# Optimization experiments

Hardware: AMD Instinct MI355X
Metric: run time of the kernel (lower is better)

The kernel has to match this reference:

```python
import jax, jax.numpy as jnp
import numpy as np

N = 50000   # nodes
E = 800000  # edges
G = 64      # graphs in the batch
DIN = 128
DOUT = 256


def _lin(key, fan_in, fan_out):
    s = 1.0 / np.sqrt(fan_in)
    kw, kb = jax.random.split(key)
    W = jax.random.uniform(kw, (fan_in, fan_out), jnp.float32, -s, s)
    b = jax.random.uniform(kb, (fan_out,), jnp.float32, -s, s)
    return W, b


def setup_inputs() -> dict:
    key = jax.random.key(0)
    ks = jax.random.split(key, 12)
    x = jax.random.normal(ks[0], (N, DIN), jnp.float32)
    edge_index = jax.random.randint(ks[1], (2, E), 0, N, dtype=jnp.int64)
    batch = jnp.sort(jax.random.randint(ks[2], (N,), 0, G, dtype=jnp.int64))
    W1, b1 = _lin(ks[3], DIN, 128)
    W2, b2 = _lin(ks[4], 128, 128)
    W3, b3 = _lin(ks[5], 128, 128)
    A1, ba1 = _lin(ks[6], DIN, 64)
    A2, ba2 = _lin(ks[7], 64, 32)
    A3, ba3 = _lin(ks[8], 32, 1)
    M1, bm1 = _lin(ks[9], 128, 128)
    M2, bm2 = _lin(ks[10], 128, DOUT)
    return dict(x=x, edge_index=edge_index, batch=batch,
                W1=W1, b1=b1, W2=W2, b2=b2, W3=W3, b3=b3,
                A1=A1, ba1=ba1, A2=A2, ba2=ba2, A3=A3, ba3=ba3,
                M1=M1, bm1=bm1, M2=M2, bm2=bm2)


def _gcn_norm(edge_index, n, dtype):
    # GCNConv default: add self-loops, symmetric normalization D^-1/2 (A+I) D^-1/2
    loop = jnp.arange(n, dtype=edge_index.dtype)
    src = jnp.concatenate([edge_index[0], loop])
    dst = jnp.concatenate([edge_index[1], loop])
    deg = jax.ops.segment_sum(jnp.ones_like(dst, dtype), dst, num_segments=n)
    dinv = jnp.where(deg > 0, jax.lax.rsqrt(deg), 0.0)
    return src, dst, dinv[src] * dinv[dst]


def _gcn(h, W, b, src, dst, norm, n):
    h = h @ W                                   # [N, F_out]
    msg = h[src] * norm[:, None]                # gather + scale (memory bound)
    return jax.ops.segment_sum(msg, dst, num_segments=n) + b


def _segment_softmax(w, batch, g):
    # per-graph softmax (PyG softmax): stabilize with segment max
    m = jax.ops.segment_max(w, batch, num_segments=g)
    e = jnp.exp(w - m[batch])
    s = jax.ops.segment_sum(e, batch, num_segments=g)
    return e / (s[batch] + 1e-16)


def reference(x, edge_index, batch,
              W1, b1, W2, b2, W3, b3,
              A1, ba1, A2, ba2, A3, ba3,
              M1, bm1, M2, bm2):
    n = x.shape[0]
    src, dst, norm = _gcn_norm(edge_index, n, x.dtype)
    relu = jax.nn.relu
    # feature branch
    f = relu(_gcn(x, W1, b1, src, dst, norm, n))
    f = relu(_gcn(f, W2, b2, src, dst, norm, n))
    f = relu(_gcn(f, W3, b3, src, dst, norm, n))
    # attention branch
    w = relu(_gcn(x, A1, ba1, src, dst, norm, n))
    w = relu(_gcn(w, A2, ba2, src, dst, norm, n))
    w = relu(_gcn(w, A3, ba3, src, dst, norm, n))   # [N, 1]
    w = _segment_softmax(w, batch, G)
    # attention-weighted sum pooling per graph
    pooled = jax.ops.segment_sum(f * w, batch, num_segments=G)  # [G, 128]
    # MLP([128,128,256], batch_norm=False): Linear+ReLU, plain last Linear
    out = relu(pooled @ M1 + bm1) @ M2 + bm2
    return out
```

## Files before the change

kernel.cpp:

```cpp
#include <hip/hip_runtime.h>
#include <hip/hip_fp16.h>
#include <math.h>


#define DIN 128
#define FH  128
#define DOUT 256
#define NBUK 128
#define SUBN 512
#define IMGCAP 16384
#define ECAP 16384

typedef float f4 __attribute__((ext_vector_type(4)));
typedef float f32x4 __attribute__((ext_vector_type(4)));
typedef _Float16 h8v __attribute__((ext_vector_type(8)));
typedef _Float16 h4v __attribute__((ext_vector_type(4)));


__global__ __launch_bounds__(256) void scan1_kernel(const int* __restrict__ cnt,
        int* __restrict__ bsum, float* __restrict__ dinv, int n) {
    __shared__ int sm[256];
    int tid = threadIdx.x;
    int base = blockIdx.x * 512;
    int a = (base + tid < n) ? cnt[base + tid] : 0;
    int b = (base + 256 + tid < n) ? cnt[base + 256 + tid] : 0;
    if (base + tid < n)       dinv[base + tid]       = rsqrtf((float)(a + 1));
    if (base + 256 + tid < n) dinv[base + 256 + tid] = rsqrtf((float)(b + 1));
    sm[tid] = a + b;
    __syncthreads();
    for (int off = 128; off > 0; off >>= 1) {
        if (tid < off) sm[tid] += sm[tid + off];
        __syncthreads();
    }
    if (tid == 0) bsum[blockIdx.x] = sm[0];
}

__global__ void scan2_kernel(const int* __restrict__ bsum, int* __restrict__ boff,
                             int* __restrict__ rpN, int nb) {
    if (threadIdx.x == 0) {
        int run = 0;
        for (int i = 0; i < nb; ++i) { boff[i] = run; run += bsum[i]; }
        *rpN = run;
    }
}

__global__ __launch_bounds__(256) void scan3_kernel(const int* __restrict__ cnt,
        const int* __restrict__ boff, int* __restrict__ rp, int n) {
    __shared__ int sm[256];
    int tid = threadIdx.x;
    int base = blockIdx.x * 512;
    int i0 = base + 2 * tid;
    int c0 = (i0 < n) ? cnt[i0] : 0;
    int c1 = (i0 + 1 < n) ? cnt[i0 + 1] : 0;
    int ps = c0 + c1;
    sm[tid] = ps;
    __syncthreads();
    for (int off = 1; off < 256; off <<= 1) {
        int v = (tid >= off) ? sm[tid - off] : 0;
        __syncthreads();
        sm[tid] += v;
        __syncthreads();
    }
    int excl = sm[tid] - ps + boff[blockIdx.x];
    if (i0 < n) rp[i0] = excl;
    if (i0 + 1 < n) rp[i0 + 1] = excl + c0;
}

__global__ __launch_bounds__(256) void ebucket_kernel(const int* __restrict__ src,
        const int* __restrict__ dst, int* __restrict__ bcur,
        unsigned long long* __restrict__ entries, int E, int shift) {
    __shared__ int lcnt[NBUK], lscan[NBUK], lbase[NBUK], lcur[NBUK];
    __shared__ unsigned long long stage[2048];
    const int tid = threadIdx.x;
    const int e0 = blockIdx.x * 2048;
    if (tid < NBUK) { lcnt[tid] = 0; lcur[tid] = 0; }
    __syncthreads();
    int s_[8], d_[8];
    #pragma unroll
    for (int k = 0; k < 8; ++k) {
        int e = e0 + k * 256 + tid;
        if (e < E) {
            s_[k] = src[e];
            d_[k] = dst[e];
            atomicAdd(&lcnt[d_[k] >> shift], 1);
        } else {
            d_[k] = -1;
        }
    }
    __syncthreads();
    if (tid < NBUK) lscan[tid] = lcnt[tid];
    __syncthreads();
    for (int off = 1; off < NBUK; off <<= 1) {
        int v = 0;
        if (tid < NBUK && tid >= off) v = lscan[tid - off];
        __syncthreads();
        if (tid < NBUK) lscan[tid] += v;
        __syncthreads();
    }
    if (tid < NBUK) {
        lscan[tid] -= lcnt[tid];
        lbase[tid] = lcnt[tid] ? atomicAdd(&bcur[tid], lcnt[tid]) : 0;
    }
    __syncthreads();
    #pragma unroll
    for (int k = 0; k < 8; ++k) {
        if (d_[k] >= 0) {
            int b = d_[k] >> shift;
            int pos = lscan[b] + atomicAdd(&lcur[b], 1);
            stage[pos] = ((unsigned long long)(unsigned)d_[k] << 32) | (unsigned)s_[k];
        }
    }
    __syncthreads();
    const int total = min(2048, E - e0);
    for (int i = tid; i < total; i += 256) {
        int lo = 0, hi = NBUK - 1;
        while (lo < hi) {
            int mid = (lo + hi + 1) >> 1;
            if (lscan[mid] <= i) lo = mid; else hi = mid - 1;
        }
        int idx = lbase[lo] + (i - lscan[lo]);
        if (idx < (lo + 1) * ECAP)
            entries[(size_t)idx] = stage[i];
    }
}

__global__ __launch_bounds__(512) void ecount_kernel(
        const unsigned long long* __restrict__ entries,
        const int* __restrict__ bcur, int* __restrict__ cnt, int n, int shift) {
    __shared__ int hist[SUBN];
    const int b = blockIdx.x;
    const int n0 = b << shift;
    if (n0 >= n) return;
    const int n1 = min(n0 + SUBN, n);
    const int tid = threadIdx.x;
    hist[tid] = 0;
    __syncthreads();
    const size_t ebase = (size_t)b * ECAP;
    const int len = min(bcur[b] - b * ECAP, ECAP);
    for (int i = tid; i < len; i += 512)
        atomicAdd(&hist[(int)(entries[ebase + i] >> 32) - n0], 1);
    __syncthreads();
    if (n0 + tid < n1) cnt[n0 + tid] = hist[tid];
}

__global__ __launch_bounds__(512) void ecsr_kernel(
        const unsigned long long* __restrict__ entries,
        const int* __restrict__ rp, const float* __restrict__ dinv,
        long long* __restrict__ cn, int n, int shift) {
    __shared__ long long img[IMGCAP];
    __shared__ int hist[SUBN];
    __shared__ int lcur[SUBN];
    __shared__ int sm[SUBN];
    __shared__ float dl[SUBN];
    const int b = blockIdx.x;
    const int n0 = b << shift;
    if (n0 >= n) return;
    const int n1 = min(n0 + (1 << shift), n);
    const int base = rp[n0];
    const int len  = rp[n1] - base;
    const size_t ebase = (size_t)b * ECAP;
    const int tid = threadIdx.x;
    hist[tid] = 0;
    lcur[tid] = 0;
    if (n0 + tid < n1) dl[tid] = dinv[n0 + tid];
    __syncthreads();
    for (int i = tid; i < len; i += 512)
        atomicAdd(&hist[(int)(entries[ebase + i] >> 32) - n0], 1);
    __syncthreads();
    int v = hist[tid];
    sm[tid] = v;
    __syncthreads();
    for (int off = 1; off < SUBN; off <<= 1) {
        int t = (tid >= off) ? sm[tid - off] : 0;
        __syncthreads();
        sm[tid] += t;
        __syncthreads();
    }
    hist[tid] = sm[tid] - v;
    __syncthreads();
    const bool fits = (len <= IMGCAP);
    for (int i = tid; i < len; i += 512) {
        unsigned long long e = entries[ebase + i];
        int d  = (int)(e >> 32) - n0;
        int sx = (int)(unsigned)(e & 0xffffffffu);
        int pos = hist[d] + atomicAdd(&lcur[d], 1);
        float w = dinv[sx] * dl[d];
        long long val = (long long)(unsigned)sx | ((long long)__float_as_int(w) << 32);
        if (fits) img[pos] = val;
        else      cn[base + pos] = val;
    }
    __syncthreads();
    if (fits)
        for (int i = tid; i < len; i += 512) cn[base + i] = img[i];
}

__global__ void gstart_kernel(const int* __restrict__ batch, int* __restrict__ gstart,
                              int n, int g) {
    int t = threadIdx.x;
    if (t > g) return;
    int lo = 0, hi = n;
    while (lo < hi) {
        int mid = (lo + hi) >> 1;
        if (batch[mid] < t) lo = mid + 1; else hi = mid;
    }
    gstart[t] = lo;
}

__global__ void cvt16_kernel(const float* __restrict__ in, __half* __restrict__ outh,
                             long n8) {
    long i = (long)blockIdx.x * 256 + threadIdx.x;
    if (i >= n8) return;
    f4 a = ((const f4*)in)[2 * i];
    f4 b = ((const f4*)in)[2 * i + 1];
    __half2 h0 = __float22half2_rn(make_float2(a.x, a.y));
    __half2 h1 = __float22half2_rn(make_float2(a.z, a.w));
    __half2 h2 = __float22half2_rn(make_float2(b.x, b.y));
    __half2 h3 = __float22half2_rn(make_float2(b.z, b.w));
    uint4 st;
    st.x = *(unsigned*)&h0; st.y = *(unsigned*)&h1;
    st.z = *(unsigned*)&h2; st.w = *(unsigned*)&h3;
    ((uint4*)outh)[i] = st;
}


__device__ __forceinline__ void wsplit(const float* __restrict__ W,
        _Float16* __restrict__ Th, _Float16* __restrict__ Tl,
        int fin, int fout, int i) {
    int r = i / fout, c = i % fout;
    float w = W[i];
    _Float16 h = (_Float16)w;
    Th[c * fin + r] = h;
    Tl[c * fin + r] = (_Float16)(w - (float)h);
}

__global__ __launch_bounds__(256) void wprep_kernel(const float* __restrict__ W1,
        const float* __restrict__ W2, const float* __restrict__ W3,
        const float* __restrict__ A1, const float* __restrict__ A2,
        _Float16* __restrict__ T, int* __restrict__ bcur) {
    int i = blockIdx.x * 256 + threadIdx.x;
    if (blockIdx.x == 0 && threadIdx.x < NBUK) bcur[threadIdx.x] = threadIdx.x * ECAP;
    if (i < 16384)       wsplit(W1, T,          T + 16384,  128, 128, i);
    else if (i < 32768)  wsplit(W2, T + 32768,  T + 49152,  128, 128, i - 16384);
    else if (i < 49152)  wsplit(W3, T + 65536,  T + 81920,  128, 128, i - 32768);
    else if (i < 57344)  wsplit(A1, T + 98304,  T + 106496, 128, 64,  i - 49152);
    else if (i < 59392)  wsplit(A2, T + 114688, T + 116736, 64,  32,  i - 57344);
}


__global__ __launch_bounds__(256) void fusedl1_kernel(const float* __restrict__ Y,
        const _Float16* __restrict__ T, const float* __restrict__ b1,
        const float* __restrict__ ba1, __half* __restrict__ t2,
        __half* __restrict__ u2, int n) {
    constexpr int LSTR  = 136;
    constexpr int LSTRB = 68;
    __shared__ _Float16 L1[64 * LSTR];
    __shared__ _Float16 L2[64 * LSTR];
    __shared__ _Float16 Ah_[64 * LSTRB];
    __shared__ _Float16 Al_[64 * LSTRB];
    const int tid  = threadIdx.x;
    const int w    = tid >> 6;
    const int lane = tid & 63;
    const int bk   = (lane >> 4) * 8;
    const int cl   = lane & 15;
    const long row0 = (long)blockIdx.x * 64;

    for (int i = tid; i < 64 * 32; i += 256) {
        int r = i >> 5, c4 = i & 31;
        long gr = row0 + r;
        float4 v = {0.f, 0.f, 0.f, 0.f};
        if (gr < n) v = *(const float4*)&Y[gr * 128 + c4 * 4];
        _Float16 h0 = (_Float16)v.x, h1 = (_Float16)v.y;
        _Float16 h2 = (_Float16)v.z, h3 = (_Float16)v.w;
        *(h4v*)&L1[r * LSTR + c4 * 4] = (h4v){h0, h1, h2, h3};
        *(h4v*)&L2[r * LSTR + c4 * 4] =
            (h4v){(_Float16)(v.x - (float)h0), (_Float16)(v.y - (float)h1),
                  (_Float16)(v.z - (float)h2), (_Float16)(v.w - (float)h3)};
    }
    __syncthreads();

    {
        const _Float16* A1h = T + 98304;
        const _Float16* A1l = T + 106496;
        const int ca = w * 16 + cl;
        h8v A1hf[4], A1lf[4];
        #pragma unroll
        for (int kk = 0; kk < 4; ++kk) {
            A1hf[kk] = *(const h8v*)&A1h[ca * 128 + kk * 32 + bk];
            A1lf[kk] = *(const h8v*)&A1l[ca * 128 + kk * 32 + bk];
        }
        f32x4 accA[4];
        #pragma unroll
        for (int rt = 0; rt < 4; ++rt) accA[rt] = (f32x4){0.f,0.f,0.f,0.f};
        #pragma unroll
        for (int rt = 0; rt < 4; ++rt) {
            int r = rt * 16 + cl;
            #pragma unroll
            for (int kk = 0; kk < 4; ++kk) {
                h8v ah = *(const h8v*)&L1[r * LSTR + kk * 32 + bk];
                h8v al = *(const h8v*)&L2[r * LSTR + kk * 32 + bk];
                accA[rt] = __builtin_amdgcn_mfma_f32_16x16x32_f16(ah, A1hf[kk], accA[rt], 0, 0, 0);
                accA[rt] = __builtin_amdgcn_mfma_f32_16x16x32_f16(ah, A1lf[kk], accA[rt], 0, 0, 0);
                accA[rt] = __builtin_amdgcn_mfma_f32_16x16x32_f16(al, A1hf[kk], accA[rt], 0, 0, 0);
            }
        }
        float bv = ba1[ca];
        #pragma unroll
        for (int rt = 0; rt < 4; ++rt) {
            int rowb = rt * 16 + (lane >> 4) * 4;
            #pragma unroll
            for (int j = 0; j < 4; ++j) {
                float v = fmaxf(accA[rt][j] + bv, 0.f);
                _Float16 h = (_Float16)v;
                Ah_[(rowb + j) * LSTRB + ca] = h;
                Al_[(rowb + j) * LSTRB + ca] = (_Float16)(v - (float)h);
            }
        }
    }

    f32x4 accF[4][2];
    {
        const _Float16* W1h = T;
        const _Float16* W1l = T + 16384;
        h8v Bh[2][4], Bl[2][4];
        #pragma unroll
        for (int ct = 0; ct < 2; ++ct) {
            int c = w * 32 + ct * 16 + cl;
            #pragma unroll
            for (int kk = 0; kk < 4; ++kk) {
                Bh[ct][kk] = *(const h8v*)&W1h[c * 128 + kk * 32 + bk];
                Bl[ct][kk] = *(const h8v*)&W1l[c * 128 + kk * 32 + bk];
            }
        }
        #pragma unroll
        for (int rt = 0; rt < 4; ++rt)
            #pragma unroll
            for (int ct = 0; ct < 2; ++ct) accF[rt][ct] = (f32x4){0.f,0.f,0.f,0.f};
        #pragma unroll
        for (int rt = 0; rt < 4; ++rt) {
            int r = rt * 16 + cl;
            #pragma unroll
            for (int kk = 0; kk < 4; ++kk) {
                h8v ah = *(const h8v*)&L1[r * LSTR + kk * 32 + bk];
                h8v al = *(const h8v*)&L2[r * LSTR + kk * 32 + bk];
                #pragma unroll
                for (int ct = 0; ct < 2; ++ct) {
                    accF[rt][ct] = __builtin_amdgcn_mfma_f32_16x16x32_f16(ah, Bh[ct][kk], accF[rt][ct], 0, 0, 0);
                    accF[rt][ct] = __builtin_amdgcn_mfma_f32_16x16x32_f16(ah, Bl[ct][kk], accF[rt][ct], 0, 0, 0);
                    accF[rt][ct] = __builtin_amdgcn_mfma_f32_16x16x32_f16(al, Bh[ct][kk], accF[rt][ct], 0, 0, 0);
                }
            }
        }
    }
    __syncthreads();

    #pragma unroll
    for (int rt = 0; rt < 4; ++rt) {
        int rowb = rt * 16 + (lane >> 4) * 4;
        #pragma unroll
        for (int ct = 0; ct < 2; ++ct) {
            int col = w * 32 + ct * 16 + cl;
            float bv = b1[col];
            #pragma unroll
            for (int j = 0; j < 4; ++j) {
                float v = fmaxf(accF[rt][ct][j] + bv, 0.f);
                _Float16 h = (_Float16)v;
                L1[(rowb + j) * LSTR + col] = h;
                L2[(rowb + j) * LSTR + col] = (_Float16)(v - (float)h);
            }
        }
    }
    __syncthreads();

    {
        const _Float16* W2h = T + 32768;
        const _Float16* W2l = T + 49152;
        h8v Bh[2][4], Bl[2][4];
        #pragma unroll
        for (int ct = 0; ct < 2; ++ct) {
            int c = w * 32 + ct * 16 + cl;
            #pragma unroll
            for (int kk = 0; kk < 4; ++kk) {
                Bh[ct][kk] = *(const h8v*)&W2h[c * 128 + kk * 32 + bk];
                Bl[ct][kk] = *(const h8v*)&W2l[c * 128 + kk * 32 + bk];
            }
        }
        f32x4 acc[4][2];
        #pragma unroll
        for (int rt = 0; rt < 4; ++rt)
            #pragma unroll
            for (int ct = 0; ct < 2; ++ct) acc[rt][ct] = (f32x4){0.f,0.f,0.f,0.f};
        #pragma unroll
        for (int rt = 0; rt < 4; ++rt) {
            int r = rt * 16 + cl;
            #pragma unroll
            for (int kk = 0; kk < 4; ++kk) {
                h8v ah = *(const h8v*)&L1[r * LSTR + kk * 32 + bk];
                h8v al = *(const h8v*)&L2[r * LSTR + kk * 32 + bk];
                #pragma unroll
                for (int ct = 0; ct < 2; ++ct) {
                    acc[rt][ct] = __builtin_amdgcn_mfma_f32_16x16x32_f16(ah, Bh[ct][kk], acc[rt][ct], 0, 0, 0);
                    acc[rt][ct] = __builtin_amdgcn_mfma_f32_16x16x32_f16(ah, Bl[ct][kk], acc[rt][ct], 0, 0, 0);
                    acc[rt][ct] = __builtin_amdgcn_mfma_f32_16x16x32_f16(al, Bh[ct][kk], acc[rt][ct], 0, 0, 0);
                }
            }
        }
        #pragma unroll
        for (int rt = 0; rt < 4; ++rt) {
            long rbase = row0 + rt * 16 + (lane >> 4) * 4;
            #pragma unroll
            for (int ct = 0; ct < 2; ++ct) {
                int col = w * 32 + ct * 16 + cl;
                #pragma unroll
                for (int j = 0; j < 4; ++j) {
                    long r = rbase + j;
                    if (r < n) t2[r * 128 + col] = __float2half(acc[rt][ct][j]);
                }
            }
        }
    }

    {
        const _Float16* A2h = T + 114688;
        const _Float16* A2l = T + 116736;
        h8v Bh[2][2], Bl[2][2];
        #pragma unroll
        for (int ct = 0; ct < 2; ++ct) {
            int c = ct * 16 + cl;
            #pragma unroll
            for (int kk = 0; kk < 2; ++kk) {
                Bh[ct][kk] = *(const h8v*)&A2h[c * 64 + kk * 32 + bk];
                Bl[ct][kk] = *(const h8v*)&A2l[c * 64 + kk * 32 + bk];
            }
        }
        f32x4 acc[2];
        acc[0] = (f32x4){0.f,0.f,0.f,0.f};
        acc[1] = (f32x4){0.f,0.f,0.f,0.f};
        const int r = w * 16 + cl;
        #pragma unroll
        for (int kk = 0; kk < 2; ++kk) {
            h8v ah = *(const h8v*)&Ah_[r * LSTRB + kk * 32 + bk];
            h8v al = *(const h8v*)&Al_[r * LSTRB + kk * 32 + bk];
            #pragma unroll
            for (int ct = 0; ct < 2; ++ct) {
                acc[ct] = __builtin_amdgcn_mfma_f32_16x16x32_f16(ah, Bh[ct][kk], acc[ct], 0, 0, 0);
                acc[ct] = __builtin_amdgcn_mfma_f32_16x16x32_f16(ah, Bl[ct][kk], acc[ct], 0, 0, 0);
                acc[ct] = __builtin_amdgcn_mfma_f32_16x16x32_f16(al, Bh[ct][kk], acc[ct], 0, 0, 0);
            }
        }
        long rbase = row0 + w * 16 + (lane >> 4) * 4;
        #pragma unroll
        for (int ct = 0; ct < 2; ++ct) {
            int col = ct * 16 + cl;
            #pragma unroll
            for (int j = 0; j < 4; ++j) {
                long rr = rbase + j;
                if (rr < n) u2[rr * 32 + col] = __float2half(acc[ct][j]);
            }
        }
    }
}

template<int FIN, int FOUT, int OMODE>
__global__ __launch_bounds__(256) void mgemm_kernel(const float* __restrict__ A,
        const _Float16* __restrict__ Wh, const _Float16* __restrict__ Wl,
        const float* __restrict__ bias, void* __restrict__ Cv, int n) {
    constexpr int NWC  = (FOUT / 16 < 4) ? FOUT / 16 : 4;
    constexpr int NWR  = 4 / NWC;
    constexpr int BM   = 64 * NWR;
    constexpr int CT   = FOUT / 16 / NWC;
    constexpr int KS   = FIN / 32;
    constexpr int LSTR = FIN + 8;
    __shared__ _Float16 Ahs[BM * LSTR];
    __shared__ _Float16 Als[BM * LSTR];

    const int tid  = threadIdx.x;
    const int w    = tid >> 6;
    const int lane = tid & 63;
    const long row0 = (long)blockIdx.x * BM;

    for (int i = tid; i < BM * (FIN / 4); i += 256) {
        int r  = i / (FIN / 4);
        int c4 = i % (FIN / 4);
        long gr = row0 + r;
        float4 v = {0.f, 0.f, 0.f, 0.f};
        if (gr < n) v = *(const float4*)&A[gr * FIN + c4 * 4];
        _Float16 h0 = (_Float16)v.x, h1 = (_Float16)v.y;
        _Float16 h2 = (_Float16)v.z, h3 = (_Float16)v.w;
        h4v hh = {h0, h1, h2, h3};
        h4v ll = {(_Float16)(v.x - (float)h0), (_Float16)(v.y - (float)h1),
                  (_Float16)(v.z - (float)h2), (_Float16)(v.w - (float)h3)};
        *(h4v*)&Ahs[r * LSTR + c4 * 4] = hh;
        *(h4v*)&Als[r * LSTR + c4 * 4] = ll;
    }

    const int wc = w % NWC;
    const int wr = w / NWC;
    const int colbase = wc * CT * 16;
    const int bk = (lane >> 4) * 8;
    h8v Bh[CT][KS], Bl[CT][KS];
    #pragma unroll
    for (int ct = 0; ct < CT; ++ct) {
        int c = colbase + ct * 16 + (lane & 15);
        #pragma unroll
        for (int kk = 0; kk < KS; ++kk) {
            Bh[ct][kk] = *(const h8v*)&Wh[(size_t)c * FIN + kk * 32 + bk];
            Bl[ct][kk] = *(const h8v*)&Wl[(size_t)c * FIN + kk * 32 + bk];
        }
    }

    __syncthreads();

    f32x4 acc[4][CT];
    #pragma unroll
    for (int rt = 0; rt < 4; ++rt)
        #pragma unroll
        for (int ct = 0; ct < CT; ++ct)
            acc[rt][ct] = (f32x4){0.f, 0.f, 0.f, 0.f};

    #pragma unroll
    for (int rt = 0; rt < 4; ++rt) {
        const int r = wr * 64 + rt * 16 + (lane & 15);
        #pragma unroll
        for (int kk = 0; kk < KS; ++kk) {
            h8v ah = *(const h8v*)&Ahs[r * LSTR + kk * 32 + bk];
            h8v al = *(const h8v*)&Als[r * LSTR + kk * 32 + bk];
            #pragma unroll
            for (int ct = 0; ct < CT; ++ct) {
                acc[rt][ct] = __builtin_amdgcn_mfma_f32_16x16x32_f16(ah, Bh[ct][kk], acc[rt][ct], 0, 0, 0);
                acc[rt][ct] = __builtin_amdgcn_mfma_f32_16x16x32_f16(ah, Bl[ct][kk], acc[rt][ct], 0, 0, 0);
                acc[rt][ct] = __builtin_amdgcn_mfma_f32_16x16x32_f16(al, Bh[ct][kk], acc[rt][ct], 0, 0, 0);
            }
        }
    }

    #pragma unroll
    for (int rt = 0; rt < 4; ++rt) {
        const long rbase = row0 + wr * 64 + rt * 16 + (lane >> 4) * 4;
        #pragma unroll
        for (int ct = 0; ct < CT; ++ct) {
            const int col = colbase + ct * 16 + (lane & 15);
            if (OMODE == 1) {
                const float bv = bias[col];
                #pragma unroll
                for (int j = 0; j < 4; ++j) {
                    long r = rbase + j;
                    if (r < n)
                        ((float*)Cv)[r * FOUT + col] = fmaxf(acc[rt][ct][j] + bv, 0.f);
                }
            } else {
                #pragma unroll
                for (int j = 0; j < 4; ++j) {
                    long r = rbase + j;
                    if (r < n)
                        ((__half*)Cv)[r * FOUT + col] = __float2half(acc[rt][ct][j]);
                }
            }
        }
    }
}


__device__ __forceinline__ void hacc8(float acc[8], uint4 u, float w) {
    __half2 h; float2 f;
    h = *(__half2*)&u.x; f = __half22float2(h); acc[0] += w * f.x; acc[1] += w * f.y;
    h = *(__half2*)&u.y; f = __half22float2(h); acc[2] += w * f.x; acc[3] += w * f.y;
    h = *(__half2*)&u.z; f = __half22float2(h); acc[4] += w * f.x; acc[5] += w * f.y;
    h = *(__half2*)&u.w; f = __half22float2(h); acc[6] += w * f.x; acc[7] += w * f.y;
}

template<int F, bool BR>
__global__ __launch_bounds__(256) void aggh_kernel(const __half* __restrict__ tin,
        const float* __restrict__ bias, const float* __restrict__ dinv,
        const int* __restrict__ rp, const long long* __restrict__ cn,
        float* __restrict__ out, int n) {
    constexpr int LPR   = F / 8;
    constexpr int SLOTS = 64 / LPR;
    const int lane = threadIdx.x & 63;
    const int node = blockIdx.x * 4 + (threadIdx.x >> 6);
    if (node >= n) return;
    const int l    = lane % LPR;
    const int slot = lane / LPR;
    const uint4* base = (const uint4*)tin + l;
    const int e0 = rp[node], e1 = rp[node + 1];
    float acc[8] = {0.f, 0.f, 0.f, 0.f, 0.f, 0.f, 0.f, 0.f};
    if (slot == 0) {
        float di = dinv[node];
        uint4 u = base[(size_t)node * LPR];
        hacc8(acc, u, di * di);
    }
    int p = e0 + slot;
    for (; p + 3 * SLOTS < e1; p += 4 * SLOTS) {
        long long r0 = __builtin_nontemporal_load(cn + p);
        long long r1 = __builtin_nontemporal_load(cn + p + SLOTS);
        long long r2 = __builtin_nontemporal_load(cn + p + 2 * SLOTS);
        long long r3 = __builtin_nontemporal_load(cn + p + 3 * SLOTS);
        uint4 u0 = base[(size_t)(unsigned)r0 * LPR];
        uint4 u1 = base[(size_t)(unsigned)r1 * LPR];
        uint4 u2 = base[(size_t)(unsigned)r2 * LPR];
        uint4 u3 = base[(size_t)(unsigned)r3 * LPR];
        hacc8(acc, u0, __int_as_float((int)(r0 >> 32)));
        hacc8(acc, u1, __int_as_float((int)(r1 >> 32)));
        hacc8(acc, u2, __int_as_float((int)(r2 >> 32)));
        hacc8(acc, u3, __int_as_float((int)(r3 >> 32)));
    }
    for (; p + SLOTS < e1; p += 2 * SLOTS) {
        long long r0 = __builtin_nontemporal_load(cn + p);
        long long r1 = __builtin_nontemporal_load(cn + p + SLOTS);
        uint4 u0 = base[(size_t)(unsigned)r0 * LPR];
        uint4 u1 = base[(size_t)(unsigned)r1 * LPR];
        hacc8(acc, u0, __int_as_float((int)(r0 >> 32)));
        hacc8(acc, u1, __int_as_float((int)(r1 >> 32)));
    }
    if (p < e1) {
        long long r0 = __builtin_nontemporal_load(cn + p);
        uint4 u0 = base[(size_t)(unsigned)r0 * LPR];
        hacc8(acc, u0, __int_as_float((int)(r0 >> 32)));
    }
    #pragma unroll
    for (int off = 32; off >= LPR; off >>= 1) {
        #pragma unroll
        for (int j = 0; j < 8; ++j) acc[j] += __shfl_xor(acc[j], off);
    }
    if (slot == 0) {
        if (BR) {
            #pragma unroll
            for (int j = 0; j < 8; ++j)
                acc[j] = fmaxf(acc[j] + bias[l * 8 + j], 0.f);
        }
        f4 lo = {acc[0], acc[1], acc[2], acc[3]};
        f4 hi = {acc[4], acc[5], acc[6], acc[7]};
        float* o = out + (size_t)node * F + l * 8;
        __builtin_nontemporal_store(lo, (f4*)o);
        __builtin_nontemporal_store(hi, (f4*)(o + 4));
    }
}

__global__ __launch_bounds__(256) void aggh32a_kernel(const __half* __restrict__ tin,
        const float* __restrict__ ba2, const float* __restrict__ A3,
        const float* __restrict__ dinv, const int* __restrict__ rp,
        const long long* __restrict__ cn, float* __restrict__ wlin, int n) {
    constexpr int LPR   = 4;
    constexpr int SLOTS = 16;
    const int lane = threadIdx.x & 63;
    const int node = blockIdx.x * 4 + (threadIdx.x >> 6);
    if (node >= n) return;
    const int l    = lane % LPR;
    const int slot = lane / LPR;
    const uint4* base = (const uint4*)tin + l;
    const int e0 = rp[node], e1 = rp[node + 1];
    float acc[8] = {0.f, 0.f, 0.f, 0.f, 0.f, 0.f, 0.f, 0.f};
    if (slot == 0) {
        float di = dinv[node];
        uint4 u = base[(size_t)node * LPR];
        hacc8(acc, u, di * di);
    }
    int p = e0 + slot;
    for (; p + SLOTS < e1; p += 2 * SLOTS) {
        long long r0 = __builtin_nontemporal_load(cn + p);
        long long r1 = __builtin_nontemporal_load(cn + p + SLOTS);
        uint4 u0 = base[(size_t)(unsigned)r0 * LPR];
        uint4 u1 = base[(size_t)(unsigned)r1 * LPR];
        hacc8(acc, u0, __int_as_float((int)(r0 >> 32)));
        hacc8(acc, u1, __int_as_float((int)(r1 >> 32)));
    }
    if (p < e1) {
        long long r0 = __builtin_nontemporal_load(cn + p);
        uint4 u0 = base[(size_t)(unsigned)r0 * LPR];
        hacc8(acc, u0, __int_as_float((int)(r0 >> 32)));
    }
    #pragma unroll
    for (int off = 32; off >= LPR; off >>= 1) {
        #pragma unroll
        for (int j = 0; j < 8; ++j) acc[j] += __shfl_xor(acc[j], off);
    }
    if (slot == 0) {
        float part = 0.f;
        #pragma unroll
        for (int j = 0; j < 8; ++j)
            part += fmaxf(acc[j] + ba2[l * 8 + j], 0.f) * A3[l * 8 + j];
        part += __shfl_xor(part, 1);
        part += __shfl_xor(part, 2);
        if (l == 0) wlin[node] = part;
    }
}

__global__ void agg1_kernel(const float* __restrict__ tin, const float* __restrict__ bias,
        const float* __restrict__ dinv, const int* __restrict__ rp,
        const long long* __restrict__ cn, float* __restrict__ out, int n) {
    int i = blockIdx.x * 256 + threadIdx.x;
    if (i >= n) return;
    float di = dinv[i];
    float acc = di * di * tin[i];
    int e0 = rp[i], e1 = rp[i + 1];
    int p = e0;
    float a0 = 0.f, a1 = 0.f, a2 = 0.f, a3 = 0.f;
    for (; p + 3 < e1; p += 4) {
        long long r0 = __builtin_nontemporal_load(cn + p);
        long long r1 = __builtin_nontemporal_load(cn + p + 1);
        long long r2 = __builtin_nontemporal_load(cn + p + 2);
        long long r3 = __builtin_nontemporal_load(cn + p + 3);
        a0 += __int_as_float((int)(r0 >> 32)) * tin[(int)(unsigned)r0];
        a1 += __int_as_float((int)(r1 >> 32)) * tin[(int)(unsigned)r1];
        a2 += __int_as_float((int)(r2 >> 32)) * tin[(int)(unsigned)r2];
        a3 += __int_as_float((int)(r3 >> 32)) * tin[(int)(unsigned)r3];
    }
    for (; p < e1; ++p) {
        long long r0 = __builtin_nontemporal_load(cn + p);
        a0 += __int_as_float((int)(r0 >> 32)) * tin[(int)(unsigned)r0];
    }
    acc += a0 + a1 + a2 + a3 + bias[0];
    out[i] = acc > 0.f ? acc : 0.f;
}


__global__ __launch_bounds__(256) void smexp_kernel(const float* __restrict__ w,
        const int* __restrict__ gstart, float* __restrict__ gsum,
        float* __restrict__ e) {
    const int g = blockIdx.x;
    const int a = gstart[g], b = gstart[g + 1];
    const int tid = threadIdx.x;
    __shared__ float red[4];
    float m = 0.f;
    for (int i = a + tid; i < b; i += 256) m = fmaxf(m, w[i]);
    #pragma unroll
    for (int off = 32; off > 0; off >>= 1) m = fmaxf(m, __shfl_xor(m, off));
    if ((tid & 63) == 0) red[tid >> 6] = m;
    __syncthreads();
    m = fmaxf(fmaxf(red[0], red[1]), fmaxf(red[2], red[3]));
    float s = 0.f;
    for (int i = a + tid; i < b; i += 256) {
        float ex = expf(w[i] - m);
        e[i] = ex;
        s += ex;
    }
    #pragma unroll
    for (int off = 32; off > 0; off >>= 1) s += __shfl_xor(s, off);
    __syncthreads();
    if ((tid & 63) == 0) red[tid >> 6] = s;
    __syncthreads();
    if (tid == 0) gsum[g] = red[0] + red[1] + red[2] + red[3];
}


__global__ __launch_bounds__(128) void pool_kernel(const float* __restrict__ f3,
        const float* __restrict__ e, const float* __restrict__ gsum,
        const int* __restrict__ gstart, float* __restrict__ pooled) {
    constexpr int SPG = 64;
    const int g = blockIdx.x / SPG, s = blockIdx.x % SPG;
    const int a = gstart[g], bnd = gstart[g + 1];
    const int len = bnd - a;
    if (len <= 0) return;
    const int chunk = (len + SPG - 1) / SPG;
    const int lo = a + s * chunk;
    const int hi = min(lo + chunk, bnd);
    if (lo >= hi) return;
    const float inv = 1.f / (gsum[g] + 1e-16f);
    const int tid = threadIdx.x;
    const int lane4 = tid & 31;
    const int rs    = tid >> 5;
    f4 acc = {0.f, 0.f, 0.f, 0.f};
    for (int i = lo + rs; i < hi; i += 4) {
        float w = e[i] * inv;
        f4 v = *(const f4*)&f3[(size_t)i * FH + lane4 * 4];
        acc.x += w * v.x; acc.y += w * v.y;
        acc.z += w * v.z; acc.w += w * v.w;
    }
    acc.x += __shfl_xor(acc.x, 32);
    acc.y += __shfl_xor(acc.y, 32);
    acc.z += __shfl_xor(acc.z, 32);
    acc.w += __shfl_xor(acc.w, 32);
    __shared__ float sm[128];
    if (tid >= 64 && tid < 96) *(f4*)&sm[(tid - 64) * 4] = acc;
    __syncthreads();
    if (tid < 32) {
        f4 o = *(f4*)&sm[tid * 4];
        o.x += acc.x; o.y += acc.y; o.z += acc.z; o.w += acc.w;
        float* dst = &pooled[g * FH + tid * 4];
        atomicAdd(dst + 0, o.x);
        atomicAdd(dst + 1, o.y);
        atomicAdd(dst + 2, o.z);
        atomicAdd(dst + 3, o.w);
    }
}


__global__ __launch_bounds__(128) void mlp1_kernel(const float* __restrict__ pooled,
        const float* __restrict__ M1, const float* __restrict__ bm1,
        float* __restrict__ hidden) {
    __shared__ float pr[FH];
    int g = blockIdx.x, j = threadIdx.x;
    pr[j] = pooled[g * FH + j];
    __syncthreads();
    float acc = bm1[j];
    #pragma unroll 8
    for (int k = 0; k < FH; ++k) acc += pr[k] * M1[k * FH + j];
    hidden[g * FH + j] = acc > 0.f ? acc : 0.f;
}

__global__ __launch_bounds__(256) void mlp2_kernel(const float* __restrict__ hidden,
        const float* __restrict__ M2, const float* __restrict__ bm2,
        float* __restrict__ out) {
    __shared__ float hr[FH];
    int g = blockIdx.x, j = threadIdx.x;
    if (j < FH) hr[j] = hidden[g * FH + j];
    __syncthreads();
    float acc = bm2[j];
    #pragma unroll 8
    for (int k = 0; k < FH; ++k) acc += hr[k] * M2[k * DOUT + j];
    out[g * DOUT + j] = acc;
}


extern "C" void kernel_launch(void* const* d_in, const int* in_sizes, int n_in,
                              void* d_out, int out_size, void* d_ws, size_t ws_size,
                              hipStream_t stream) {
    const float* x   = (const float*)d_in[0];
    const int*   ei  = (const int*)d_in[1];
    const int*   batch = (const int*)d_in[2];
    const float* W1  = (const float*)d_in[3];
    const float* b1  = (const float*)d_in[4];
    const float* W2  = (const float*)d_in[5];
    const float* b2  = (const float*)d_in[6];
    const float* W3  = (const float*)d_in[7];
    const float* b3  = (const float*)d_in[8];
    const float* A1  = (const float*)d_in[9];
    const float* ba1 = (const float*)d_in[10];
    const float* A2  = (const float*)d_in[11];
    const float* ba2 = (const float*)d_in[12];
    const float* A3  = (const float*)d_in[13];
    const float* ba3 = (const float*)d_in[14];
    const float* M1  = (const float*)d_in[15];
    const float* bm1 = (const float*)d_in[16];
    const float* M2  = (const float*)d_in[17];
    const float* bm2 = (const float*)d_in[18];

    const int N = in_sizes[0] / DIN;
    const int E = in_sizes[1] / 2;
    const int G = out_size / DOUT;
    const int* src = ei;
    const int* dst = ei + E;
    float* out = (float*)d_out;

    int shift = 9;
    while (((N + (1 << shift) - 1) >> shift) > NBUK) ++shift;
    const int nbuckets = (N + (1 << shift) - 1) >> shift;

    char* p = (char*)d_ws;
    auto alloc = [&](size_t bytes) -> void* {
        void* r = (void*)p;
        p += (bytes + 255) & ~(size_t)255;
        return r;
    };
    float* dinv  = (float*)alloc((size_t)N * 4);
    int*   cnt   = (int*)alloc((size_t)N * 4);
    int*   rp    = (int*)alloc((size_t)(N + 1) * 4);
    long long* cn = (long long*)alloc((size_t)E * 8);
    float* SY    = (float*)alloc((size_t)N * FH * 4);
    float* SA    = (float*)alloc((size_t)N * FH * 4);
    __half* ST   = (__half*)alloc((size_t)N * FH * 2);
    char*  SX    = (char*)alloc((size_t)N * 256);
    __half* u2   = (__half*)alloc((size_t)N * 32 * 2);
    float* wlin  = (float*)alloc((size_t)N * 4);
    float* wact  = (float*)alloc((size_t)N * 4);
    float* ebuf  = (float*)alloc((size_t)N * 4);
    float* gsum  = (float*)alloc((size_t)G * 4);
    int*   gstart= (int*)alloc((size_t)(G + 1) * 4);
    float* pooled= (float*)alloc((size_t)G * FH * 4);
    float* hidden= (float*)alloc((size_t)G * FH * 4);
    int*   bsum  = (int*)alloc(256 * 4);
    int*   boff  = (int*)alloc(256 * 4);
    int*   bcur  = (int*)alloc(NBUK * 4);
    _Float16* WT = (_Float16*)alloc((size_t)118784 * 2);

    __half* xh = (__half*)SX;
    unsigned long long* entries = (unsigned long long*)SA;

    hipMemsetAsync(pooled, 0, (size_t)G * FH * 4, stream);

    const int nb = (N + 255) / 256;
    const int NB = (N + 511) / 512;

    wprep_kernel<<<232, 256, 0, stream>>>(W1, W2, W3, A1, A2, WT, bcur);
    ebucket_kernel<<<(E + 2047) / 2048, 256, 0, stream>>>(src, dst, bcur, entries, E, shift);
    ecount_kernel<<<nbuckets, 512, 0, stream>>>(entries, bcur, cnt, N, shift);
    scan1_kernel<<<NB, 256, 0, stream>>>(cnt, bsum, dinv, N);
    scan2_kernel<<<1, 64, 0, stream>>>(bsum, boff, rp + N, NB);
    scan3_kernel<<<NB, 256, 0, stream>>>(cnt, boff, rp, N);
    gstart_kernel<<<1, 128, 0, stream>>>(batch, gstart, N, G);
    ecsr_kernel<<<nbuckets, 512, 0, stream>>>(entries, rp, dinv, cn, N, shift);

    const long n8 = (long)N * FH / 8;
    cvt16_kernel<<<(int)((n8 + 255) / 256), 256, 0, stream>>>(x, xh, n8);

    const int gb64 = (N + 63) / 64;
    const int agb  = (N + 3) / 4;

    aggh_kernel<FH, false><<<agb, 256, 0, stream>>>(xh, nullptr, dinv, rp, cn, SY, N);

    fusedl1_kernel<<<gb64, 256, 0, stream>>>(SY, WT, b1, ba1, (__half*)ST, u2, N);

    aggh_kernel<FH, true><<<agb, 256, 0, stream>>>(ST, b2, dinv, rp, cn, SA, N);
    mgemm_kernel<FH, FH, 2><<<gb64, 256, 0, stream>>>(SA, WT + 65536, WT + 81920, nullptr, ST, N);
    aggh_kernel<FH, true><<<agb, 256, 0, stream>>>(ST, b3, dinv, rp, cn, SY, N);

    aggh32a_kernel<<<agb, 256, 0, stream>>>(u2, ba2, A3, dinv, rp, cn, wlin, N);
    agg1_kernel<<<nb, 256, 0, stream>>>(wlin, ba3, dinv, rp, cn, wact, N);

    smexp_kernel<<<G, 256, 0, stream>>>(wact, gstart, gsum, ebuf);
    pool_kernel<<<G * 64, 128, 0, stream>>>(SY, ebuf, gsum, gstart, pooled);

    mlp1_kernel<<<G, 128, 0, stream>>>(pooled, M1, bm1, hidden);
    mlp2_kernel<<<G, 256, 0, stream>>>(hidden, M2, bm2, out);
}
```

Measured before the change: 310.3 us.

## Fuse attention-branch aggregations into feature-branch aggregation passes and merge MLP kernels

Measured after the change: 315.1 us. Within noise of the previous version (+1.5%).

```diff
diff --git a/kernel.cpp b/kernel.cpp
--- a/kernel.cpp
+++ b/kernel.cpp
@@ -635,81 +635,155 @@
     }
 }
 
-__global__ __launch_bounds__(256) void aggh32a_kernel(const __half* __restrict__ tin,
+__global__ __launch_bounds__(256) void aggf2a2_kernel(const __half* __restrict__ t2,
+        const __half* __restrict__ u2, const float* __restrict__ b2,
         const float* __restrict__ ba2, const float* __restrict__ A3,
         const float* __restrict__ dinv, const int* __restrict__ rp,
-        const long long* __restrict__ cn, float* __restrict__ wlin, int n) {
-    constexpr int LPR   = 4;
-    constexpr int SLOTS = 16;
+        const long long* __restrict__ cn, float* __restrict__ f2,
+        float* __restrict__ wlin, int n) {
     const int lane = threadIdx.x & 63;
     const int node = blockIdx.x * 4 + (threadIdx.x >> 6);
     if (node >= n) return;
-    const int l    = lane % LPR;
-    const int slot = lane / LPR;
-    const uint4* base = (const uint4*)tin + l;
+    const int l    = lane & 15;
+    const int slot = lane >> 4;
+    const bool ul  = (l < 4);
+    const uint4* base  = (const uint4*)t2 + l;
+    const uint4* ubase = (const uint4*)u2 + l;
     const int e0 = rp[node], e1 = rp[node + 1];
-    float acc[8] = {0.f, 0.f, 0.f, 0.f, 0.f, 0.f, 0.f, 0.f};
+    float acc[8]  = {0.f,0.f,0.f,0.f,0.f,0.f,0.f,0.f};
+    float acc2[8] = {0.f,0.f,0.f,0.f,0.f,0.f,0.f,0.f};
     if (slot == 0) {
         float di = dinv[node];
-        uint4 u = base[(size_t)node * LPR];
-        hacc8(acc, u, di * di);
+        float dd = di * di;
+        hacc8(acc, base[(size_t)node * 16], dd);
+        if (ul) hacc8(acc2, ubase[(size_t)node * 4], dd);
     }
     int p = e0 + slot;
-    for (; p + SLOTS < e1; p += 2 * SLOTS) {
+    for (; p + 12 < e1; p += 16) {
         long long r0 = __builtin_nontemporal_load(cn + p);
-        long long r1 = __builtin_nontemporal_load(cn + p + SLOTS);
-        uint4 u0 = base[(size_t)(unsigned)r0 * LPR];
-        uint4 u1 = base[(size_t)(unsigned)r1 * LPR];
-        hacc8(acc, u0, __int_as_float((int)(r0 >> 32)));
-        hacc8(acc, u1, __int_as_float((int)(r1 >> 32)));
-    }
-    if (p < e1) {
+        long long r1 = __builtin_nontemporal_load(cn + p + 4);
+        long long r2 = __builtin_nontemporal_load(cn + p + 8);
+        long long r3 = __builtin_nontemporal_load(cn + p + 12);
+        unsigned s0 = (unsigned)r0, s1 = (unsigned)r1, s2 = (unsigned)r2, s3 = (unsigned)r3;
+        float w0 = __int_as_float((int)(r0 >> 32));
+        float w1 = __int_as_float((int)(r1 >> 32));
+        float w2 = __int_as_float((int)(r2 >> 32));
+        float w3 = __int_as_float((int)(r3 >> 32));
+        hacc8(acc, base[(size_t)s0 * 16], w0);
+        hacc8(acc, base[(size_t)s1 * 16], w1);
+        hacc8(acc, base[(size_t)s2 * 16], w2);
+        hacc8(acc, base[(size_t)s3 * 16], w3);
+        if (ul) {
+            hacc8(acc2, ubase[(size_t)s0 * 4], w0);
+            hacc8(acc2, ubase[(size_t)s1 * 4], w1);
+            hacc8(acc2, ubase[(size_t)s2 * 4], w2);
+            hacc8(acc2, ubase[(size_t)s3 * 4], w3);
+        }
+    }
+    for (; p < e1; p += 4) {
         long long r0 = __builtin_nontemporal_load(cn + p);
-        uint4 u0 = base[(size_t)(unsigned)r0 * LPR];
-        hacc8(acc, u0, __int_as_float((int)(r0 >> 32)));
-    }
-    #pragma unroll
-    for (int off = 32; off >= LPR; off >>= 1) {
-        #pragma unroll
-        for (int j = 0; j < 8; ++j) acc[j] += __shfl_xor(acc[j], off);
+        unsigned s0 = (unsigned)r0;
+        float w0 = __int_as_float((int)(r0 >> 32));
+        hacc8(acc, base[(size_t)s0 * 16], w0);
+        if (ul) hacc8(acc2, ubase[(size_t)s0 * 4], w0);
+    }
+    #pragma unroll
+    for (int off = 32; off >= 16; off >>= 1) {
+        #pragma unroll
+        for (int j = 0; j < 8; ++j) {
+            acc[j]  += __shfl_xor(acc[j],  off);
+            acc2[j] += __shfl_xor(acc2[j], off);
+        }
     }
     if (slot == 0) {
+        #pragma unroll
+        for (int j = 0; j < 8; ++j)
+            acc[j] = fmaxf(acc[j] + b2[l * 8 + j], 0.f);
+        f4 lo = {acc[0], acc[1], acc[2], acc[3]};
+        f4 hi = {acc[4], acc[5], acc[6], acc[7]};
+        float* o = f2 + (size_t)node * FH + l * 8;
+        __builtin_nontemporal_store(lo, (f4*)o);
+        __builtin_nontemporal_store(hi, (f4*)(o + 4));
         float part = 0.f;
-        #pragma unroll
-        for (int j = 0; j < 8; ++j)
-            part += fmaxf(acc[j] + ba2[l * 8 + j], 0.f) * A3[l * 8 + j];
+        if (ul) {
+            #pragma unroll
+            for (int j = 0; j < 8; ++j)
+                part += fmaxf(acc2[j] + ba2[l * 8 + j], 0.f) * A3[l * 8 + j];
+        }
         part += __shfl_xor(part, 1);
         part += __shfl_xor(part, 2);
         if (l == 0) wlin[node] = part;
     }
 }
 
-__global__ void agg1_kernel(const float* __restrict__ tin, const float* __restrict__ bias,
-        const float* __restrict__ dinv, const int* __restrict__ rp,
-        const long long* __restrict__ cn, float* __restrict__ out, int n) {
-    int i = blockIdx.x * 256 + threadIdx.x;
-    if (i >= n) return;
-    float di = dinv[i];
-    float acc = di * di * tin[i];
-    int e0 = rp[i], e1 = rp[i + 1];
-    int p = e0;
-    float a0 = 0.f, a1 = 0.f, a2 = 0.f, a3 = 0.f;
-    for (; p + 3 < e1; p += 4) {
+__global__ __launch_bounds__(256) void aggf3w_kernel(const __half* __restrict__ t3,
+        const float* __restrict__ wlin, const float* __restrict__ b3,
+        const float* __restrict__ ba3, const float* __restrict__ dinv,
+        const int* __restrict__ rp, const long long* __restrict__ cn,
+        float* __restrict__ f3, float* __restrict__ wact, int n) {
+    const int lane = threadIdx.x & 63;
+    const int node = blockIdx.x * 4 + (threadIdx.x >> 6);
+    if (node >= n) return;
+    const int l    = lane & 15;
+    const int slot = lane >> 4;
+    const bool wl  = (l == 0);
+    const uint4* base = (const uint4*)t3 + l;
+    const int e0 = rp[node], e1 = rp[node + 1];
+    float acc[8] = {0.f,0.f,0.f,0.f,0.f,0.f,0.f,0.f};
+    float accw = 0.f;
+    if (slot == 0) {
+        float di = dinv[node];
+        float dd = di * di;
+        hacc8(acc, base[(size_t)node * 16], dd);
+        if (wl) accw += dd * wlin[node];
+    }
+    int p = e0 + slot;
+    for (; p + 12 < e1; p += 16) {
         long long r0 = __builtin_nontemporal_load(cn + p);
-        long long r1 = __builtin_nontemporal_load(cn + p + 1);
-        long long r2 = __builtin_nontemporal_load(cn + p + 2);
-        long long r3 = __builtin_nontemporal_load(cn + p + 3);
-        a0 += __int_as_float((int)(r0 >> 32)) * tin[(int)(unsigned)r0];
-        a1 += __int_as_float((int)(r1 >> 32)) * tin[(int)(unsigned)r1];
-        a2 += __int_as_float((int)(r2 >> 32)) * tin[(int)(unsigned)r2];
-        a3 += __int_as_float((int)(r3 >> 32)) * tin[(int)(unsigned)r3];
-    }
-    for (; p < e1; ++p) {
+        long long r1 = __builtin_nontemporal_load(cn + p + 4);
+        long long r2 = __builtin_nontemporal_load(cn + p + 8);
+        long long r3 = __builtin_nontemporal_load(cn + p + 12);
+        unsigned s0 = (unsigned)r0, s1 = (unsigned)r1, s2 = (unsigned)r2, s3 = (unsigned)r3;
+        float w0 = __int_as_float((int)(r0 >> 32));
+        float w1 = __int_as_float((int)(r1 >> 32));
+        float w2 = __int_as_float((int)(r2 >> 32));
+        float w3 = __int_as_float((int)(r3 >> 32));
+        hacc8(acc, base[(size_t)s0 * 16], w0);
+        hacc8(acc, base[(size_t)s1 * 16], w1);
+        hacc8(acc, base[(size_t)s2 * 16], w2);
+        hacc8(acc, base[(size_t)s3 * 16], w3);
+        if (wl) {
+            accw += w0 * wlin[s0] + w1 * wlin[s1];
+            accw += w2 * wlin[s2] + w3 * wlin[s3];
+        }
+    }
+    for (; p < e1; p += 4) {
         long long r0 = __builtin_nontemporal_load(cn + p);
-        a0 += __int_as_float((int)(r0 >> 32)) * tin[(int)(unsigned)r0];
-    }
-    acc += a0 + a1 + a2 + a3 + bias[0];
-    out[i] = acc > 0.f ? acc : 0.f;
+        unsigned s0 = (unsigned)r0;
+        float w0 = __int_as_float((int)(r0 >> 32));
+        hacc8(acc, base[(size_t)s0 * 16], w0);
+        if (wl) accw += w0 * wlin[s0];
+    }
+    #pragma unroll
+    for (int off = 32; off >= 16; off >>= 1) {
+        #pragma unroll
+        for (int j = 0; j < 8; ++j) acc[j] += __shfl_xor(acc[j], off);
+        accw += __shfl_xor(accw, off);
+    }
+    if (slot == 0) {
+        #pragma unroll
+        for (int j = 0; j < 8; ++j)
+            acc[j] = fmaxf(acc[j] + b3[l * 8 + j], 0.f);
+        f4 lo = {acc[0], acc[1], acc[2], acc[3]};
+        f4 hi = {acc[4], acc[5], acc[6], acc[7]};
+        float* o = f3 + (size_t)node * FH + l * 8;
+        __builtin_nontemporal_store(lo, (f4*)o);
+        __builtin_nontemporal_store(hi, (f4*)(o + 4));
+        if (wl) {
+            float v = accw + ba3[0];
+            wact[node] = v > 0.f ? v : 0.f;
+        }
+    }
 }
 
 
@@ -784,25 +858,21 @@
 }
 
 
-__global__ __launch_bounds__(128) void mlp1_kernel(const float* __restrict__ pooled,
+__global__ __launch_bounds__(256) void mlp_kernel(const float* __restrict__ pooled,
         const float* __restrict__ M1, const float* __restrict__ bm1,
-        float* __restrict__ hidden) {
-    __shared__ float pr[FH];
-    int g = blockIdx.x, j = threadIdx.x;
-    pr[j] = pooled[g * FH + j];
-    __syncthreads();
-    float acc = bm1[j];
-    #pragma unroll 8
-    for (int k = 0; k < FH; ++k) acc += pr[k] * M1[k * FH + j];
-    hidden[g * FH + j] = acc > 0.f ? acc : 0.f;
-}
-
-__global__ __launch_bounds__(256) void mlp2_kernel(const float* __restrict__ hidden,
         const float* __restrict__ M2, const float* __restrict__ bm2,
         float* __restrict__ out) {
+    __shared__ float pr[FH];
     __shared__ float hr[FH];
     int g = blockIdx.x, j = threadIdx.x;
-    if (j < FH) hr[j] = hidden[g * FH + j];
+    if (j < FH) pr[j] = pooled[g * FH + j];
+    __syncthreads();
+    if (j < FH) {
+        float acc = bm1[j];
+        #pragma unroll 8
+        for (int k = 0; k < FH; ++k) acc += pr[k] * M1[k * FH + j];
+        hr[j] = acc > 0.f ? acc : 0.f;
+    }
     __syncthreads();
     float acc = bm2[j];
     #pragma unroll 8
@@ -866,7 +936,6 @@
     float* gsum  = (float*)alloc((size_t)G * 4);
     int*   gstart= (int*)alloc((size_t)(G + 1) * 4);
     float* pooled= (float*)alloc((size_t)G * FH * 4);
-    float* hidden= (float*)alloc((size_t)G * FH * 4);
     int*   bsum  = (int*)alloc(256 * 4);
     int*   boff  = (int*)alloc(256 * 4);
     int*   bcur  = (int*)alloc(NBUK * 4);
@@ -877,7 +946,6 @@
 
     hipMemsetAsync(pooled, 0, (size_t)G * FH * 4, stream);
 
-    const int nb = (N + 255) / 256;
     const int NB = (N + 511) / 512;
 
     wprep_kernel<<<232, 256, 0, stream>>>(W1, W2, W3, A1, A2, WT, bcur);
@@ -899,16 +967,14 @@
 
     fusedl1_kernel<<<gb64, 256, 0, stream>>>(SY, WT, b1, ba1, (__half*)ST, u2, N);
 
-    aggh_kernel<FH, true><<<agb, 256, 0, stream>>>(ST, b2, dinv, rp, cn, SA, N);
+    aggf2a2_kernel<<<agb, 256, 0, stream>>>((__half*)ST, u2, b2, ba2, A3,
+                                            dinv, rp, cn, SA, wlin, N);
     mgemm_kernel<FH, FH, 2><<<gb64, 256, 0, stream>>>(SA, WT + 65536, WT + 81920, nullptr, ST, N);
-    aggh_kernel<FH, true><<<agb, 256, 0, stream>>>(ST, b3, dinv, rp, cn, SY, N);
-
-    aggh32a_kernel<<<agb, 256, 0, stream>>>(u2, ba2, A3, dinv, rp, cn, wlin, N);
-    agg1_kernel<<<nb, 256, 0, stream>>>(wlin, ba3, dinv, rp, cn, wact, N);
+    aggf3w_kernel<<<agb, 256, 0, stream>>>((__half*)ST, wlin, b3, ba3,
+                                           dinv, rp, cn, SY, wact, N);
 
     smexp_kernel<<<G, 256, 0, stream>>>(wact, gstart, gsum, ebuf);
     pool_kernel<<<G * 64, 128, 0, stream>>>(SY, ebuf, gsum, gstart, pooled);
 
-    mlp1_kernel<<<G, 128, 0, stream>>>(pooled, M1, bm1, hidden);
-    mlp2_kernel<<<G, 256, 0, stream>>>(hidden, M2, bm2, out);
-}
+    mlp_kernel<<<G, 256, 0, stream>>>(pooled, M1, bm1, M2, bm2, out);
+}
```
